# Performance work log

Hardware: AMD Instinct MI355X
Metric: run time of the kernel (lower is better)

Reference implementation:

```python
import jax, jax.numpy as jnp
import numpy as np

N, E, F, H, G = 50000, 600000, 128, 128, 256
EPS = 1e-5
NEG_SLOPE = 0.2


def setup_inputs() -> dict:
    key = jax.random.key(0)
    ks = jax.random.split(key, 20)
    def w(k, shape, fan_in):
        return jax.random.normal(k, shape, jnp.float32) / np.sqrt(fan_in)
    x = jax.random.normal(ks[0], (N, F), jnp.float32)
    edge_index = jax.random.randint(ks[1], (2, E), 0, N, jnp.int32)
    batch = jnp.sort(jax.random.randint(ks[2], (N,), 0, G, jnp.int32))
    return {
        "x": x, "edge_index": edge_index, "batch": batch,
        "W1": w(ks[3], (F, H), F), "b1": jnp.zeros((H,), jnp.float32),
        "g1": jnp.ones((H,), jnp.float32), "be1": jnp.zeros((H,), jnp.float32),
        "Wg": w(ks[4], (H, H), H), "att_src": w(ks[5], (H,), H),
        "att_dst": w(ks[6], (H,), H), "bg": jnp.zeros((H,), jnp.float32),
        "g2": jnp.ones((H,), jnp.float32), "be2": jnp.zeros((H,), jnp.float32),
        "W3": w(ks[7], (H, H), H), "b3": jnp.zeros((H,), jnp.float32),
        "g3": jnp.ones((H,), jnp.float32), "be3": jnp.zeros((H,), jnp.float32),
        "fw1": w(ks[8], (H, H), H), "fb1": jnp.zeros((H,), jnp.float32),
        "fw2": w(ks[9], (H, 1), H), "fb2": jnp.zeros((1,), jnp.float32),
    }


def _with_self_loops(edge_index):
    loop = jnp.arange(N, dtype=edge_index.dtype)
    src = jnp.concatenate([edge_index[0], loop])
    dst = jnp.concatenate([edge_index[1], loop])
    return src, dst


def gcn_conv(x, W, b, src, dst):
    h = x @ W                                      # [N,H]
    deg = jax.ops.segment_sum(jnp.ones_like(dst, jnp.float32), dst, num_segments=N)
    dis = jnp.where(deg > 0, jax.lax.rsqrt(jnp.maximum(deg, 1.0)), 0.0)
    norm = dis[src] * dis[dst]                     # [E+N]
    msg = h[src] * norm[:, None]
    return jax.ops.segment_sum(msg, dst, num_segments=N) + b


def gat_conv(x, W, a_src, a_dst, b, src, dst):
    # single-head PyG GATConv with self loops
    h = x @ W                                      # [N,H]
    al_s = h @ a_src                               # [N]
    al_d = h @ a_dst
    e = jax.nn.leaky_relu(al_s[src] + al_d[dst], NEG_SLOPE)   # [E+N]
    m = jax.ops.segment_max(e, dst, num_segments=N)
    ex = jnp.exp(e - m[dst])
    denom = jax.ops.segment_sum(ex, dst, num_segments=N)
    alpha = ex / denom[dst]
    out = jax.ops.segment_sum(h[src] * alpha[:, None], dst, num_segments=N)
    return out + b


def batch_norm(x, gamma, beta):
    mu = jnp.mean(x, axis=0)
    var = jnp.var(x, axis=0)
    return gamma * (x - mu) * jax.lax.rsqrt(var + EPS) + beta


def reference(x, edge_index, batch, W1, b1, g1, be1, Wg, att_src, att_dst, bg,
              g2, be2, W3, b3, g3, be3, fw1, fb1, fw2, fb2):
    src, dst = _with_self_loops(edge_index)
    h = jax.nn.relu(batch_norm(gcn_conv(x, W1, b1, src, dst), g1, be1))
    # dropout = identity (eval mode)
    h = jax.nn.relu(batch_norm(gat_conv(h, Wg, att_src, att_dst, bg, src, dst), g2, be2))
    h = jax.nn.relu(batch_norm(gcn_conv(h, W3, b3, src, dst), g3, be3))
    # global mean pool over graphs
    sums = jax.ops.segment_sum(h, batch, num_segments=G)           # [G,H]
    cnts = jax.ops.segment_sum(jnp.ones((h.shape[0],), h.dtype), batch, num_segments=G)
    pooled = sums / jnp.maximum(cnts, 1.0)[:, None]
    z = jax.nn.relu(pooled @ fw1 + fb1)
    return z @ fw2 + fb2                                            # [G,1]
```

## Files before the change

### kernel.cpp

```cpp
#include <hip/hip_runtime.h>
#include <hip/hip_fp16.h>
#include <cstdint>

#define N_NODES 50000
#define N_EDGES 600000
#define HDIM    128
#define NGRAPH  256
#define EPSBN   1e-5f
#define NEG     0.2f
#define SCAN_B  196

__device__ __forceinline__ float lrelu(float v){ return v > 0.f ? v : NEG*v; }

typedef _Float16     f16x8 __attribute__((ext_vector_type(8)));
typedef float        f32x4 __attribute__((ext_vector_type(4)));
typedef unsigned int u32x4 __attribute__((ext_vector_type(4)));

__global__ void prep_kernel(const float* __restrict__ W1, const float* __restrict__ Wg,
                            const float* __restrict__ W3, __half* __restrict__ Wt1,
                            __half* __restrict__ Wtg, __half* __restrict__ Wt3,
                            const int* __restrict__ ei, int* __restrict__ degi,
                            const int* __restrict__ batch, int* __restrict__ start){
  int b = blockIdx.x;
  if (b < 192){
    const float* W = (b < 64) ? W1 : (b < 128 ? Wg : W3);
    __half*     Wt = (b < 64) ? Wt1 : (b < 128 ? Wtg : Wt3);
    int idx = (b & 63)*256 + threadIdx.x;
    int k = idx >> 7, n = idx & 127;
    int kc = k >> 5, q = (k >> 3) & 3, j = k & 7;
    int nt = n >> 4, c16 = n & 15;
    Wt[(((kc*8 + nt)*4 + q)*16 + c16)*8 + j] = __float2half(W[idx]);
  } else if (b < 192 + 2344){
    int e = (b - 192)*256 + threadIdx.x;
    if (e < N_EDGES) atomicAdd(&degi[ei[N_EDGES + e]], 1);
  } else {
    int i = (b - 192 - 2344)*256 + threadIdx.x;
    if (i >= N_NODES) return;
    int bb = batch[i];
    int p = (i == 0) ? -1 : batch[i-1];
    for (int g = p+1; g <= bb; ++g) start[g] = i;
    if (i == N_NODES-1)
      for (int g = bb+1; g <= NGRAPH; ++g) start[g] = N_NODES;
  }
}

__global__ void scan_kernel(const int* __restrict__ degi, int2* __restrict__ seg,
                            int* __restrict__ work, float* __restrict__ dis,
                            int* __restrict__ gctr){
  __shared__ int sm[256];
  __shared__ int base;
  int t = threadIdx.x; int i = blockIdx.x*256 + t;
  int v = (i < N_NODES) ? degi[i] : 0;
  if (i < N_NODES) dis[i] = rsqrtf((float)v + 1.f);
  sm[t] = v; __syncthreads();
  for (int off = 1; off < 256; off <<= 1){
    int add = (t >= off) ? sm[t - off] : 0;
    __syncthreads();
    sm[t] += add; __syncthreads();
  }
  if (t == 255) base = atomicAdd(gctr, sm[255]);
  __syncthreads();
  if (i < N_NODES){
    int r = base + sm[t] - v;
    seg[i] = make_int2(r, v);
    work[i] = r;
  }
}
__global__ void csr_scatter(const int* __restrict__ ei, int* __restrict__ work,
                            int* __restrict__ colx){
  int e = blockIdx.x*256 + threadIdx.x;
  if (e >= N_EDGES) return;
  int s = ei[e], d = ei[N_EDGES + e];
  int pos = atomicAdd(&work[d], 1);
  colx[pos] = s;
}

template<bool BN, bool F32IN, bool ATT, bool SCALE>
__global__ __launch_bounds__(256) void gemm_mfma(const void* __restrict__ Xv,
    const __half* __restrict__ Wt,
    const float* __restrict__ S, const float* __restrict__ Q,
    const float* __restrict__ gam, const float* __restrict__ bet,
    __half* __restrict__ Yh,
    const float* __restrict__ asr, const float* __restrict__ adt,
    float* __restrict__ al_s, float* __restrict__ al_d,
    const float* __restrict__ dis){
  __shared__ _Float16 scl[128], shl[128];
  const int t    = threadIdx.x;
  if (BN){
    if (t < 128){
      float mean = S[t] * (1.f/(float)N_NODES);
      float var  = fmaxf(Q[t]*(1.f/(float)N_NODES) - mean*mean, 0.f);
      float scale = gam[t]*rsqrtf(var + EPSBN);
      float shift = bet[t] - mean*scale;
      scl[t] = (_Float16)scale;
      shl[t] = (_Float16)shift;
    }
    __syncthreads();
  }
  const int wave = t >> 6, lane = t & 63;
  const int q    = lane >> 4, c16 = lane & 15;
  const int m0   = blockIdx.x*64 + wave*16;
  const int row  = m0 + c16;
  const int arow = (row > N_NODES-1) ? N_NODES-1 : row;

  f32x4 acc[8];
#pragma unroll
  for (int i = 0; i < 8; ++i) acc[i] = (f32x4){0.f,0.f,0.f,0.f};

  const f16x8* Wt8 = (const f16x8*)Wt;

#pragma unroll
  for (int kc = 0; kc < 4; ++kc){
    const int kof = kc*32 + q*8;
    f16x8 a;
    if (F32IN){
      const float* xp = (const float*)Xv + (long)arow*128 + kof;
      float4 x0 = *(const float4*)xp;
      float4 x1 = *(const float4*)(xp + 4);
      a[0]=(_Float16)x0.x; a[1]=(_Float16)x0.y; a[2]=(_Float16)x0.z; a[3]=(_Float16)x0.w;
      a[4]=(_Float16)x1.x; a[5]=(_Float16)x1.y; a[6]=(_Float16)x1.z; a[7]=(_Float16)x1.w;
    } else {
      f16x8 raw = *(const f16x8*)((const _Float16*)Xv + (long)arow*128 + kof);
      if (BN){
        f16x8 scv = *(const f16x8*)(scl + kof);
        f16x8 shv = *(const f16x8*)(shl + kof);
#pragma unroll
        for (int i = 0; i < 8; ++i){
          _Float16 v = (_Float16)(raw[i]*scv[i] + shv[i]);
          a[i] = v > (_Float16)0 ? v : (_Float16)0;
        }
      } else {
        a = raw;
      }
    }
#pragma unroll
    for (int nt = 0; nt < 8; ++nt){
      f16x8 b = Wt8[(kc*8 + nt)*64 + lane];
      acc[nt] = __builtin_amdgcn_mfma_f32_16x16x32_f16(b, a, acc[nt], 0, 0, 0);
    }
  }
  float rs = SCALE ? dis[arow] : 1.f;
  if (row < N_NODES){
    __half* yp = Yh + (long)row*128 + q*4;
#pragma unroll
    for (int nt = 0; nt < 8; ++nt){
      union { uint2 u; __half2 h[2]; } pk;
      pk.h[0] = __floats2half2_rn(acc[nt][0]*rs, acc[nt][1]*rs);
      pk.h[1] = __floats2half2_rn(acc[nt][2]*rs, acc[nt][3]*rs);
      *(uint2*)(yp + nt*16) = pk.u;
    }
  }
  if (ATT){
    float s = 0.f, d = 0.f;
#pragma unroll
    for (int nt = 0; nt < 8; ++nt){
      float4 av = *(const float4*)(asr + nt*16 + q*4);
      float4 bv = *(const float4*)(adt + nt*16 + q*4);
      s += acc[nt][0]*av.x + acc[nt][1]*av.y + acc[nt][2]*av.z + acc[nt][3]*av.w;
      d += acc[nt][0]*bv.x + acc[nt][1]*bv.y + acc[nt][2]*bv.z + acc[nt][3]*bv.w;
    }
    s += __shfl_xor(s, 16); s += __shfl_xor(s, 32);
    d += __shfl_xor(d, 16); d += __shfl_xor(d, 32);
    if (q == 0 && row < N_NODES){ al_s[row] = s; al_d[row] = d; }
  }
}

__global__ __launch_bounds__(256) void gcn_agg(const _Float16* __restrict__ Ah,
    const float* __restrict__ dis, const int2* __restrict__ seg,
    const int* __restrict__ colx, __half* __restrict__ Bh){
  const int n = blockIdx.x*4 + (threadIdx.x >> 6);
  const int lane = threadIdx.x & 63;
  const int g = lane >> 4, p = lane & 15;
  float acc[8] = {0,0,0,0,0,0,0,0};
  if (g == 0){
    f16x8 self = *(const f16x8*)(Ah + (long)n*128 + p*8);
#pragma unroll
    for (int i = 0; i < 8; ++i) acc[i] = (float)self[i];
  }
  const int2 sg = seg[n];
  const int e0 = sg.x, cnt = sg.y;
  int j = g;
  for (; j + 4 < cnt; j += 8){
    int s0 = colx[e0 + j];
    int s1 = colx[e0 + j + 4];
    f16x8 r0 = *(const f16x8*)(Ah + (long)s0*128 + p*8);
    f16x8 r1 = *(const f16x8*)(Ah + (long)s1*128 + p*8);
#pragma unroll
    for (int i = 0; i < 8; ++i) acc[i] += (float)r0[i];
#pragma unroll
    for (int i = 0; i < 8; ++i) acc[i] += (float)r1[i];
  }
  if (j < cnt){
    int s0 = colx[e0 + j];
    f16x8 r0 = *(const f16x8*)(Ah + (long)s0*128 + p*8);
#pragma unroll
    for (int i = 0; i < 8; ++i) acc[i] += (float)r0[i];
  }
#pragma unroll
  for (int i = 0; i < 8; ++i){
    acc[i] += __shfl_xor(acc[i], 16);
    acc[i] += __shfl_xor(acc[i], 32);
  }
  if (g == 0){
    float dn = dis[n];
    union { u32x4 u; __half2 h[4]; } pk;
#pragma unroll
    for (int i = 0; i < 4; ++i)
      pk.h[i] = __floats2half2_rn(acc[2*i]*dn, acc[2*i+1]*dn);
    __builtin_nontemporal_store(pk.u, (u32x4*)(Bh + (long)n*128 + p*8));
  }
}

__global__ __launch_bounds__(256) void gat_agg(const _Float16* __restrict__ Ah,
    const float* __restrict__ al_s, const float* __restrict__ al_d,
    const int2* __restrict__ seg, const int* __restrict__ colx,
    __half* __restrict__ Bh){
  const int n = blockIdx.x*4 + (threadIdx.x >> 6);
  const int lane = threadIdx.x & 63;
  const int g = lane >> 4, p = lane & 15;
  const float adn = al_d[n];
  const float lself = lrelu(al_s[n] + adn);
  const int2 sg = seg[n];
  const int e0 = sg.x, cnt = sg.y;
  float m = lself;
  for (int idx = lane; idx < cnt; idx += 64)
    m = fmaxf(m, lrelu(al_s[colx[e0 + idx]] + adn));
#pragma unroll
  for (int off = 32; off; off >>= 1) m = fmaxf(m, __shfl_xor(m, off));
  const float exs = __expf(lself - m);
  float acc[8] = {0,0,0,0,0,0,0,0};
  if (g == 0){
    f16x8 self = *(const f16x8*)(Ah + (long)n*128 + p*8);
#pragma unroll
    for (int i = 0; i < 8; ++i) acc[i] = exs * (float)self[i];
  }
  float dpart = 0.f;
  int j = g;
  for (; j + 4 < cnt; j += 8){
    int s0 = colx[e0 + j];
    int s1 = colx[e0 + j + 4];
    float w0 = __expf(lrelu(al_s[s0] + adn) - m);
    float w1 = __expf(lrelu(al_s[s1] + adn) - m);
    f16x8 r0 = *(const f16x8*)(Ah + (long)s0*128 + p*8);
    f16x8 r1 = *(const f16x8*)(Ah + (long)s1*128 + p*8);
    dpart += w0 + w1;
#pragma unroll
    for (int i = 0; i < 8; ++i) acc[i] += w0 * (float)r0[i];
#pragma unroll
    for (int i = 0; i < 8; ++i) acc[i] += w1 * (float)r1[i];
  }
  if (j < cnt){
    int s0 = colx[e0 + j];
    float w0 = __expf(lrelu(al_s[s0] + adn) - m);
    f16x8 r0 = *(const f16x8*)(Ah + (long)s0*128 + p*8);
    dpart += w0;
#pragma unroll
    for (int i = 0; i < 8; ++i) acc[i] += w0 * (float)r0[i];
  }
  dpart += __shfl_xor(dpart, 16);
  dpart += __shfl_xor(dpart, 32);
#pragma unroll
  for (int i = 0; i < 8; ++i){
    acc[i] += __shfl_xor(acc[i], 16);
    acc[i] += __shfl_xor(acc[i], 32);
  }
  if (g == 0){
    float rinv = 1.f / (dpart + exs);
    union { u32x4 u; __half2 h[4]; } pk;
#pragma unroll
    for (int i = 0; i < 4; ++i)
      pk.h[i] = __floats2half2_rn(acc[2*i]*rinv, acc[2*i+1]*rinv);
    __builtin_nontemporal_store(pk.u, (u32x4*)(Bh + (long)n*128 + p*8));
  }
}

__global__ void stats_h(const f16x8* __restrict__ X8,
                        float* __restrict__ S, float* __restrict__ Q){
  __shared__ float sb[16][16][8];
  __shared__ float qb[16][16][8];
  int t = threadIdx.x;
  int cg = t & 15, r = t >> 4;
  float s[8] = {0,0,0,0,0,0,0,0}, q[8] = {0,0,0,0,0,0,0,0};
  const int total = N_NODES*16;
  for (int idx = blockIdx.x*256 + t; idx < total; idx += gridDim.x*256){
    f16x8 v = X8[idx];
#pragma unroll
    for (int i = 0; i < 8; ++i){
      float f = (float)v[i];
      s[i] += f; q[i] += f*f;
    }
  }
#pragma unroll
  for (int i = 0; i < 8; ++i){ sb[r][cg][i] = s[i]; qb[r][cg][i] = q[i]; }
  __syncthreads();
  if (t < 128){
    int cg2 = t >> 3, j = t & 7;
    float as = 0.f, aq = 0.f;
#pragma unroll
    for (int r2 = 0; r2 < 16; ++r2){ as += sb[r2][cg2][j]; aq += qb[r2][cg2][j]; }
    atomicAdd(&S[cg2*8 + j], as);
    atomicAdd(&Q[cg2*8 + j], aq);
  }
}

__global__ void poolfinal(const __half* __restrict__ Bh, const int* __restrict__ start,
                          const float* __restrict__ S, const float* __restrict__ Q,
                          const float* __restrict__ gam, const float* __restrict__ bet,
                          const float* __restrict__ fw1, const float* __restrict__ fb1,
                          const float* __restrict__ fw2, const float* __restrict__ fb2,
                          float* __restrict__ out){
  __shared__ float scl[128], shl[128], psum[2][128], p[128], red[2];
  int t = threadIdx.x, gg = blockIdx.x;
  if (t < 128){
    float mean = S[t] * (1.f/(float)N_NODES);
    float var  = fmaxf(Q[t]*(1.f/(float)N_NODES) - mean*mean, 0.f);
    float scale = gam[t]*rsqrtf(var + EPSBN);
    scl[t] = scale;
    shl[t] = bet[t] - mean*scale;
  }
  __syncthreads();
  int s0 = start[gg], s1 = start[gg+1];
  int c = t & 127, h = t >> 7;
  float acc = 0.f;
  for (int n = s0 + h; n < s1; n += 2)
    acc += fmaxf(__half2float(Bh[(long)n*128 + c])*scl[c] + shl[c], 0.f);
  psum[h][c] = acc;
  __syncthreads();
  if (t < 128){
    float cnt = fmaxf((float)(s1 - s0), 1.f);
    p[t] = (psum[0][t] + psum[1][t]) / cnt;
  }
  __syncthreads();
  if (t < 128){
    float a = fb1[t];
    for (int k = 0; k < 128; ++k) a += p[k]*fw1[k*128 + t];
    float z = fmaxf(a, 0.f) * fw2[t];
    for (int off = 32; off; off >>= 1) z += __shfl_down(z, off);
    if ((t & 63) == 0) red[t >> 6] = z;
  }
  __syncthreads();
  if (t == 0) out[gg] = red[0] + red[1] + fb2[0];
}

extern "C" void kernel_launch(void* const* d_in, const int* in_sizes, int n_in,
                              void* d_out, int out_size, void* d_ws, size_t ws_size,
                              hipStream_t stream){
  const float* x    = (const float*)d_in[0];
  const int*   ei   = (const int*)d_in[1];
  const int*   batch= (const int*)d_in[2];
  const float* W1   = (const float*)d_in[3];
  const float* g1   = (const float*)d_in[5];
  const float* be1  = (const float*)d_in[6];
  const float* Wg   = (const float*)d_in[7];
  const float* asr  = (const float*)d_in[8];
  const float* adt  = (const float*)d_in[9];
  const float* g2   = (const float*)d_in[11];
  const float* be2  = (const float*)d_in[12];
  const float* W3   = (const float*)d_in[13];
  const float* g3   = (const float*)d_in[15];
  const float* be3  = (const float*)d_in[16];
  const float* fw1  = (const float*)d_in[17];
  const float* fb1  = (const float*)d_in[18];
  const float* fw2  = (const float*)d_in[19];
  const float* fb2  = (const float*)d_in[20];
  float* out = (float*)d_out;

  const long NH = (long)N_NODES*HDIM;
  __half* Ah    = (__half*)d_ws;
  __half* Bh    = Ah + NH;
  __half* Wt1   = Bh + NH;
  __half* Wtg   = Wt1 + 16384;
  __half* Wt3   = Wtg + 16384;
  float* dis    = (float*)(Wt3 + 16384);
  float* al_s   = dis + N_NODES;
  float* al_d   = al_s + N_NODES;
  int* deg_i    = (int*)(al_d + N_NODES);
  float* stats  = (float*)(deg_i + N_NODES);
  int* gctr     = (int*)(stats + 768);
  int2* seg     = (int2*)(gctr + 4);
  int* work     = (int*)(seg + N_NODES);
  int* colx     = work + N_NODES;
  int* start    = colx + N_EDGES;

  (void)hipMemsetAsync(deg_i, 0, (size_t)(N_NODES + 768 + 4) * sizeof(int), stream);

  const int TB = 256;
  const int gE  = (N_EDGES + TB - 1)/TB;
  const int gMM = (N_NODES + 63)/64;
  const int gAgg= N_NODES / 4;

  const _Float16* Ahf = (const _Float16*)Ah;
  const f16x8*    Bh8 = (const f16x8*)Bh;

  prep_kernel<<<192 + gE + SCAN_B, TB, 0, stream>>>(W1, Wg, W3, Wt1, Wtg, Wt3,
                                                    ei, deg_i, batch, start);
  scan_kernel<<<SCAN_B, TB, 0, stream>>>(deg_i, seg, work, dis, gctr);
  csr_scatter<<<gE, TB, 0, stream>>>(ei, work, colx);

  gemm_mfma<false,true,false,true><<<gMM, TB, 0, stream>>>(x, Wt1,
      nullptr, nullptr, nullptr, nullptr, Ah, nullptr, nullptr, nullptr, nullptr, dis);
  gcn_agg<<<gAgg, TB, 0, stream>>>(Ahf, dis, seg, colx, Bh);
  stats_h<<<512, TB, 0, stream>>>(Bh8, stats + 0, stats + 128);

  gemm_mfma<true,false,true,false><<<gMM, TB, 0, stream>>>(Bh, Wtg,
      stats + 0, stats + 128, g1, be1, Ah, asr, adt, al_s, al_d, nullptr);
  gat_agg<<<gAgg, TB, 0, stream>>>(Ahf, al_s, al_d, seg, colx, Bh);
  stats_h<<<512, TB, 0, stream>>>(Bh8, stats + 256, stats + 384);

  gemm_mfma<true,false,false,true><<<gMM, TB, 0, stream>>>(Bh, Wt3,
      stats + 256, stats + 384, g2, be2, Ah, nullptr, nullptr, nullptr, nullptr, dis);
  gcn_agg<<<gAgg, TB, 0, stream>>>(Ahf, dis, seg, colx, Bh);
  stats_h<<<512, TB, 0, stream>>>(Bh8, stats + 512, stats + 640);

  poolfinal<<<NGRAPH, TB, 0, stream>>>(Bh, start, stats + 512, stats + 640, g3, be3,
                                       fw1, fb1, fw2, fb2, out);
}
```

Baseline: 378.9 us.

## Assign one 16-lane group per node in aggregation kernels with online softmax

The GCN and GAT aggregation kernels now give each destination node a 16-thread group instead of a full 64-lane wavefront, so each block covers 16 nodes rather than 4. This removes the cross-group shuffle reductions and idle lanes that came with low-degree nodes (about 12 neighbours on average). GAT switches from a separate max pass plus a weighted pass to a single-pass online softmax that rescales the accumulators as the running max changes. In exchange each group walks its neighbour list serially with only two loads in flight, which reduces per-node memory parallelism, and the online rescale adds extra exp calls.

```diff
diff --git a/kernel.cpp b/kernel.cpp
--- a/kernel.cpp
+++ b/kernel.cpp
@@ -168,27 +168,23 @@
 __global__ __launch_bounds__(256) void gcn_agg(const _Float16* __restrict__ Ah,
     const float* __restrict__ dis, const int2* __restrict__ seg,
     const int* __restrict__ colx, __half* __restrict__ Bh){
-  const int n = blockIdx.x*4 + (threadIdx.x >> 6);
-  const int lane = threadIdx.x & 63;
-  const int g = lane >> 4, p = lane & 15;
-  float acc[8] = {0,0,0,0,0,0,0,0};
-  if (g == 0){
-    f16x8 self = *(const f16x8*)(Ah + (long)n*128 + p*8);
-#pragma unroll
-    for (int i = 0; i < 8; ++i) acc[i] = (float)self[i];
-  }
+  const int t = threadIdx.x;
+  const int grp = t >> 4, p = t & 15;
+  const int n = blockIdx.x*16 + grp;
   const int2 sg = seg[n];
   const int e0 = sg.x, cnt = sg.y;
-  int j = g;
-  for (; j + 4 < cnt; j += 8){
+  f16x8 self = *(const f16x8*)(Ah + (long)n*128 + p*8);
+  float acc[8];
+#pragma unroll
+  for (int i = 0; i < 8; ++i) acc[i] = (float)self[i];
+  int j = 0;
+  for (; j + 1 < cnt; j += 2){
     int s0 = colx[e0 + j];
-    int s1 = colx[e0 + j + 4];
+    int s1 = colx[e0 + j + 1];
     f16x8 r0 = *(const f16x8*)(Ah + (long)s0*128 + p*8);
     f16x8 r1 = *(const f16x8*)(Ah + (long)s1*128 + p*8);
 #pragma unroll
-    for (int i = 0; i < 8; ++i) acc[i] += (float)r0[i];
-#pragma unroll
-    for (int i = 0; i < 8; ++i) acc[i] += (float)r1[i];
+    for (int i = 0; i < 8; ++i) acc[i] += (float)r0[i] + (float)r1[i];
   }
   if (j < cnt){
     int s0 = colx[e0 + j];
@@ -196,82 +192,65 @@
 #pragma unroll
     for (int i = 0; i < 8; ++i) acc[i] += (float)r0[i];
   }
-#pragma unroll
-  for (int i = 0; i < 8; ++i){
-    acc[i] += __shfl_xor(acc[i], 16);
-    acc[i] += __shfl_xor(acc[i], 32);
-  }
-  if (g == 0){
-    float dn = dis[n];
-    union { u32x4 u; __half2 h[4]; } pk;
-#pragma unroll
-    for (int i = 0; i < 4; ++i)
-      pk.h[i] = __floats2half2_rn(acc[2*i]*dn, acc[2*i+1]*dn);
-    __builtin_nontemporal_store(pk.u, (u32x4*)(Bh + (long)n*128 + p*8));
-  }
+  float dn = dis[n];
+  union { u32x4 u; __half2 h[4]; } pk;
+#pragma unroll
+  for (int i = 0; i < 4; ++i)
+    pk.h[i] = __floats2half2_rn(acc[2*i]*dn, acc[2*i+1]*dn);
+  __builtin_nontemporal_store(pk.u, (u32x4*)(Bh + (long)n*128 + p*8));
 }
 
 __global__ __launch_bounds__(256) void gat_agg(const _Float16* __restrict__ Ah,
     const float* __restrict__ al_s, const float* __restrict__ al_d,
     const int2* __restrict__ seg, const int* __restrict__ colx,
     __half* __restrict__ Bh){
-  const int n = blockIdx.x*4 + (threadIdx.x >> 6);
-  const int lane = threadIdx.x & 63;
-  const int g = lane >> 4, p = lane & 15;
-  const float adn = al_d[n];
-  const float lself = lrelu(al_s[n] + adn);
+  const int t = threadIdx.x;
+  const int grp = t >> 4, p = t & 15;
+  const int n = blockIdx.x*16 + grp;
   const int2 sg = seg[n];
   const int e0 = sg.x, cnt = sg.y;
-  float m = lself;
-  for (int idx = lane; idx < cnt; idx += 64)
-    m = fmaxf(m, lrelu(al_s[colx[e0 + idx]] + adn));
-#pragma unroll
-  for (int off = 32; off; off >>= 1) m = fmaxf(m, __shfl_xor(m, off));
-  const float exs = __expf(lself - m);
-  float acc[8] = {0,0,0,0,0,0,0,0};
-  if (g == 0){
-    f16x8 self = *(const f16x8*)(Ah + (long)n*128 + p*8);
-#pragma unroll
-    for (int i = 0; i < 8; ++i) acc[i] = exs * (float)self[i];
-  }
-  float dpart = 0.f;
-  int j = g;
-  for (; j + 4 < cnt; j += 8){
+  const float adn = al_d[n];
+  float m = lrelu(al_s[n] + adn);
+  float denom = 1.f;
+  f16x8 self = *(const f16x8*)(Ah + (long)n*128 + p*8);
+  float acc[8];
+#pragma unroll
+  for (int i = 0; i < 8; ++i) acc[i] = (float)self[i];
+  int j = 0;
+  for (; j + 1 < cnt; j += 2){
     int s0 = colx[e0 + j];
-    int s1 = colx[e0 + j + 4];
-    float w0 = __expf(lrelu(al_s[s0] + adn) - m);
-    float w1 = __expf(lrelu(al_s[s1] + adn) - m);
+    int s1 = colx[e0 + j + 1];
+    float a0 = lrelu(al_s[s0] + adn);
+    float a1 = lrelu(al_s[s1] + adn);
     f16x8 r0 = *(const f16x8*)(Ah + (long)s0*128 + p*8);
     f16x8 r1 = *(const f16x8*)(Ah + (long)s1*128 + p*8);
-    dpart += w0 + w1;
-#pragma unroll
-    for (int i = 0; i < 8; ++i) acc[i] += w0 * (float)r0[i];
-#pragma unroll
-    for (int i = 0; i < 8; ++i) acc[i] += w1 * (float)r1[i];
+    float nm = fmaxf(m, fmaxf(a0, a1));
+    float sc = __expf(m - nm);
+    float w0 = __expf(a0 - nm);
+    float w1 = __expf(a1 - nm);
+    denom = denom*sc + w0 + w1;
+    m = nm;
+#pragma unroll
+    for (int i = 0; i < 8; ++i)
+      acc[i] = acc[i]*sc + w0*(float)r0[i] + w1*(float)r1[i];
   }
   if (j < cnt){
     int s0 = colx[e0 + j];
-    float w0 = __expf(lrelu(al_s[s0] + adn) - m);
+    float a0 = lrelu(al_s[s0] + adn);
     f16x8 r0 = *(const f16x8*)(Ah + (long)s0*128 + p*8);
-    dpart += w0;
-#pragma unroll
-    for (int i = 0; i < 8; ++i) acc[i] += w0 * (float)r0[i];
-  }
-  dpart += __shfl_xor(dpart, 16);
-  dpart += __shfl_xor(dpart, 32);
-#pragma unroll
-  for (int i = 0; i < 8; ++i){
-    acc[i] += __shfl_xor(acc[i], 16);
-    acc[i] += __shfl_xor(acc[i], 32);
-  }
-  if (g == 0){
-    float rinv = 1.f / (dpart + exs);
-    union { u32x4 u; __half2 h[4]; } pk;
-#pragma unroll
-    for (int i = 0; i < 4; ++i)
-      pk.h[i] = __floats2half2_rn(acc[2*i]*rinv, acc[2*i+1]*rinv);
-    __builtin_nontemporal_store(pk.u, (u32x4*)(Bh + (long)n*128 + p*8));
-  }
+    float nm = fmaxf(m, a0);
+    float sc = __expf(m - nm);
+    float w0 = __expf(a0 - nm);
+    denom = denom*sc + w0;
+#pragma unroll
+    for (int i = 0; i < 8; ++i) acc[i] = acc[i]*sc + w0*(float)r0[i];
+  }
+  float rinv = 1.f / denom;
+  union { u32x4 u; __half2 h[4]; } pk;
+#pragma unroll
+  for (int i = 0; i < 4; ++i)
+    pk.h[i] = __floats2half2_rn(acc[2*i]*rinv, acc[2*i+1]*rinv);
+  __builtin_nontemporal_store(pk.u, (u32x4*)(Bh + (long)n*128 + p*8));
 }
 
 __global__ void stats_h(const f16x8* __restrict__ X8,
@@ -387,7 +366,7 @@
   const int TB = 256;
   const int gE  = (N_EDGES + TB - 1)/TB;
   const int gMM = (N_NODES + 63)/64;
-  const int gAgg= N_NODES / 4;
+  const int gAggG = N_NODES / 16;
 
   const _Float16* Ahf = (const _Float16*)Ah;
   const f16x8*    Bh8 = (const f16x8*)Bh;
@@ -399,17 +378,17 @@
 
   gemm_mfma<false,true,false,true><<<gMM, TB, 0, stream>>>(x, Wt1,
       nullptr, nullptr, nullptr, nullptr, Ah, nullptr, nullptr, nullptr, nullptr, dis);
-  gcn_agg<<<gAgg, TB, 0, stream>>>(Ahf, dis, seg, colx, Bh);
+  gcn_agg<<<gAggG, TB, 0, stream>>>(Ahf, dis, seg, colx, Bh);
   stats_h<<<512, TB, 0, stream>>>(Bh8, stats + 0, stats + 128);
 
   gemm_mfma<true,false,true,false><<<gMM, TB, 0, stream>>>(Bh, Wtg,
       stats + 0, stats + 128, g1, be1, Ah, asr, adt, al_s, al_d, nullptr);
-  gat_agg<<<gAgg, TB, 0, stream>>>(Ahf, al_s, al_d, seg, colx, Bh);
+  gat_agg<<<gAggG, TB, 0, stream>>>(Ahf, al_s, al_d, seg, colx, Bh);
   stats_h<<<512, TB, 0, stream>>>(Bh8, stats + 256, stats + 384);
 
   gemm_mfma<true,false,false,true><<<gMM, TB, 0, stream>>>(Bh, Wt3,
       stats + 256, stats + 384, g2, be2, Ah, nullptr, nullptr, nullptr, nullptr, dis);
-  gcn_agg<<<gAgg, TB, 0, stream>>>(Ahf, dis, seg, colx, Bh);
+  gcn_agg<<<gAggG, TB, 0, stream>>>(Ahf, dis, seg, colx, Bh);
   stats_h<<<512, TB, 0, stream>>>(Bh8, stats + 512, stats + 640);
 
   poolfinal<<<NGRAPH, TB, 0, stream>>>(Bh, start, stats + 512, stats + 640, g3, be3,
```

Measured after the change: 366.3 us, median of 2. 3.3% less time.
